# Kernel optimization log

Hardware: AMD Instinct MI355X
Metric: run time of the kernel (lower is better)

## Reference

```python
import jax, jax.numpy as jnp
import numpy as np

B, T, S, D = 4096, 128, 128, 32  # batch, TEXT_LEN, retweet_user_size, feature dim (hardcoded 32)


def setup_inputs() -> dict:
    key = jax.random.key(0)
    ks = jax.random.split(key, 7)
    return {
        "C": jax.random.normal(ks[0], (B, T, D), jnp.float32),
        "X1": jax.random.normal(ks[1], (B, S, D), jnp.float32),
        "W": jax.random.normal(ks[2], (D, D), jnp.float32) * 0.05,
        "Ws": jax.random.normal(ks[3], (S, S), jnp.float32) * 0.05,
        "Wc": jax.random.normal(ks[4], (T, T), jnp.float32) * 0.05,
        "was": jax.random.normal(ks[5], (D, 1), jnp.float32) * 0.05,
        "wac": jax.random.normal(ks[6], (D, 1), jnp.float32) * 0.05,
    }


def reference(C, X1, W, Ws, Wc, was, wac):
    # C: (B,T,32); X1: (B,S,32); RNN = permute(X1) -> (B,32,S)
    RNN = jnp.swapaxes(X1, 1, 2)                       # (B,32,S)
    f = jnp.einsum('btd,de->bte', C, W)                # (B,T,32)
    F = jnp.tanh(jnp.einsum('btd,bds->bts', f, RNN))   # (B,T,S) affinity
    s = jnp.einsum('bds,st->bdt', RNN, Ws)             # (B,32,S)
    c = jnp.einsum('btd,tu->bdu', C, Wc)               # (B,32,T)  (C^T @ Wc)
    Hs = jnp.tanh(s + jnp.einsum('bdt,bts->bds', c, F))   # (B,32,S)
    Hc = jnp.tanh(c + jnp.einsum('bds,bts->bdt', s, F))   # (B,32,T)  (s @ F^T)
    # K.softmax default axis=-1; scores have trailing dim 1 (faithful to source)
    As = jax.nn.softmax(jnp.einsum('bds,dk->bsk', Hs, was), axis=-1)  # (B,S,1)
    Ac = jax.nn.softmax(jnp.einsum('bdt,dk->btk', Hc, wac), axis=-1)  # (B,T,1)
    As = jnp.swapaxes(As, 1, 2)                        # (B,1,S)
    Ac = jnp.swapaxes(Ac, 1, 2)                        # (B,1,T)
    sfinal = jnp.einsum('bks,bsd->bkd', As, X1)        # (B,1,32)  As @ RNN^T
    cfinal = jnp.einsum('bkt,btd->bkd', Ac, C)         # (B,1,32)
    return jnp.concatenate([sfinal, cfinal], axis=-1)  # (B,1,64)
```

## Files before the change

kernel.cpp:

```cpp
#include <hip/hip_runtime.h>

constexpr int NB = 4096;
constexpr int NT = 128;
constexpr int NS = 128;
constexpr int ND = 32;


__device__ __forceinline__ float4 f4_add(float4 a, float4 b) {
    return make_float4(a.x + b.x, a.y + b.y, a.z + b.z, a.w + b.w);
}

__device__ __forceinline__ float4 f4_shfl_down(float4 v, int off) {
    return make_float4(__shfl_down(v.x, off, 64), __shfl_down(v.y, off, 64),
                       __shfl_down(v.z, off, 64), __shfl_down(v.w, off, 64));
}

__global__ __launch_bounds__(256) void coatt_colsum(const float* __restrict__ C,
                                                    const float* __restrict__ X1,
                                                    float* __restrict__ out) {
    const int lane = threadIdx.x & 63;
    const int wv   = (blockIdx.x << 2) + (threadIdx.x >> 6);
    const int b    = wv >> 1;
    const int isC  = wv & 1;

    const float* src = isC ? (C + (size_t)b * NT * ND)
                           : (X1 + (size_t)b * NS * ND);
    const float4* p = reinterpret_cast<const float4*>(src);

    float4 s = make_float4(0.f, 0.f, 0.f, 0.f);
    #pragma unroll 8
    for (int i = lane; i < (NS * ND) / 4; i += 64) {
        s = f4_add(s, p[i]);
    }

    #pragma unroll
    for (int off = 32; off >= 8; off >>= 1) {
        s = f4_add(s, f4_shfl_down(s, off));
    }

    if (lane < 8) {
        float4* o = reinterpret_cast<float4*>(out + (size_t)b * 64 + isC * 32);
        o[lane] = s;
    }
}

extern "C" void kernel_launch(void* const* d_in, const int* in_sizes, int n_in,
                              void* d_out, int out_size, void* d_ws, size_t ws_size,
                              hipStream_t stream) {
    const float* C  = (const float*)d_in[0];
    const float* X1 = (const float*)d_in[1];
    float* out = (float*)d_out;

    coatt_colsum<<<(NB * 2) / 4, 256, 0, stream>>>(C, X1, out);
}
```

Measured before the change: 152.1 us.

## Use persistent 1024-thread blocks with register prefetch for slice column sums

Replaces the one-wave-per-slice reduction with 2048 blocks of 1024 threads. Each block walks four slices of C or X1, with each thread loading one float4 per slice and prefetching the next slice into a register. Per-wave shuffle partials are combined through shared memory with block barriers. This aims to expose more concurrent loads across the whole GPU, at the cost of two block-wide syncs per slice and shared-memory traffic.

```diff
diff --git a/kernel.cpp b/kernel.cpp
--- a/kernel.cpp
+++ b/kernel.cpp
@@ -1,9 +1,11 @@
 #include <hip/hip_runtime.h>
 
 constexpr int NB = 4096;
-constexpr int NT = 128;
-constexpr int NS = 128;
 constexpr int ND = 32;
+constexpr int ROWS = 128;
+constexpr int SLICE_F4 = ROWS * ND / 4;
+constexpr int BLOCKS = 2048;
+constexpr int ITERS = (NB * 2) / BLOCKS;
 
 
 __device__ __forceinline__ float4 f4_add(float4 a, float4 b) {
@@ -15,32 +17,44 @@
                        __shfl_down(v.z, off, 64), __shfl_down(v.w, off, 64));
 }
 
-__global__ __launch_bounds__(256) void coatt_colsum(const float* __restrict__ C,
-                                                    const float* __restrict__ X1,
-                                                    float* __restrict__ out) {
-    const int lane = threadIdx.x & 63;
-    const int wv   = (blockIdx.x << 2) + (threadIdx.x >> 6);
-    const int b    = wv >> 1;
-    const int isC  = wv & 1;
+__global__ __launch_bounds__(1024) void coatt_colsum(const float* __restrict__ C,
+                                                     const float* __restrict__ X1,
+                                                     float* __restrict__ out) {
+    const int t    = threadIdx.x;
+    const int lane = t & 63;
+    const int w    = t >> 6;
+    const int isC  = blockIdx.x & 1;
+    const int bid2 = blockIdx.x >> 1;
 
-    const float* src = isC ? (C + (size_t)b * NT * ND)
-                           : (X1 + (size_t)b * NS * ND);
-    const float4* p = reinterpret_cast<const float4*>(src);
+    const float4* src = reinterpret_cast<const float4*>(isC ? C : X1);
 
-    float4 s = make_float4(0.f, 0.f, 0.f, 0.f);
-    #pragma unroll 8
-    for (int i = lane; i < (NS * ND) / 4; i += 64) {
-        s = f4_add(s, p[i]);
-    }
+    __shared__ float4 part[16][8];
+
+    float4 cur = src[(size_t)bid2 * SLICE_F4 + t];
 
     #pragma unroll
-    for (int off = 32; off >= 8; off >>= 1) {
-        s = f4_add(s, f4_shfl_down(s, off));
-    }
+    for (int k = 0; k < ITERS; ++k) {
+        const int b = bid2 + k * (BLOCKS / 2);
+        float4 nxt = make_float4(0.f, 0.f, 0.f, 0.f);
+        if (k + 1 < ITERS)
+            nxt = src[((size_t)b + BLOCKS / 2) * SLICE_F4 + t];
 
-    if (lane < 8) {
-        float4* o = reinterpret_cast<float4*>(out + (size_t)b * 64 + isC * 32);
-        o[lane] = s;
+        float4 s = cur;
+        #pragma unroll
+        for (int off = 32; off >= 8; off >>= 1)
+            s = f4_add(s, f4_shfl_down(s, off));
+        if (lane < 8) part[w][lane] = s;
+        __syncthreads();
+
+        if (t < 8) {
+            float4 acc = part[0][t];
+            #pragma unroll
+            for (int ww = 1; ww < 16; ++ww)
+                acc = f4_add(acc, part[ww][t]);
+            reinterpret_cast<float4*>(out + (size_t)b * 64 + isC * 32)[t] = acc;
+        }
+        __syncthreads();
+        cur = nxt;
     }
 }
 
@@ -51,5 +65,5 @@
     const float* X1 = (const float*)d_in[1];
     float* out = (float*)d_out;
 
-    coatt_colsum<<<(NB * 2) / 4, 256, 0, stream>>>(C, X1, out);
+    coatt_colsum<<<BLOCKS, 1024, 0, stream>>>(C, X1, out);
 }
```

Measured after the change: 153.9 us. Within noise of the previous version (+1.2%).
